# Performance work log

Hardware: AMD Instinct MI355X
Metric: run time of the kernel (lower is better)

Reference implementation:

```python
import jax, jax.numpy as jnp
import numpy as np

B = 65536
DIM = 256       # latent_dim
N_EMBED = 1024  # codebook size


def setup_inputs() -> dict:
    key = jax.random.key(0)
    kx, ke = jax.random.split(key)
    x = jax.random.normal(kx, (B, DIM), dtype=jnp.float32)
    # rosinality Quantize stores codebook as embed[dim, n_embed]
    embed = jax.random.normal(ke, (DIM, N_EMBED), dtype=jnp.float32)
    return {"x": x, "embed": embed}


def reference(x, embed):
    # dist[b, k] = ||x_b||^2 - 2 x_b . e_k + ||e_k||^2  (negated for argmax in
    # the original; equivalent to argmin of the distance)
    x_sq = jnp.sum(x * x, axis=1, keepdims=True)            # [B, 1]
    e_sq = jnp.sum(embed * embed, axis=0, keepdims=True)    # [1, K]
    dist = x_sq - 2.0 * (x @ embed) + e_sq                  # [B, K]
    embed_ind = jnp.argmin(dist, axis=1)                    # [B] int
    # codebook lookup: embed.T is [K, dim]
    quantize = jnp.take(embed.T, embed_ind, axis=0)         # [B, dim]
    # commitment loss term
    diff = jnp.mean(jnp.square(jax.lax.stop_gradient(quantize) - x))
    # straight-through estimator
    quantize_st = x + jax.lax.stop_gradient(quantize - x)
    return quantize_st, diff, embed_ind
```

## Files before the change

### kernel.cpp

```cpp
#include <hip/hip_runtime.h>

#define NROWSQ   65536
#define NDIM     256
#define NCB      1024
#define DIFF_OFF 16777216
#define IDX_OFF  16777217

#define MARGIN_A 0.35f
#define MARGIN_B 1.5e-3f
#define SCORE_SHIFT 384.0f

typedef __attribute__((ext_vector_type(8))) short s16x8;
typedef __attribute__((ext_vector_type(4))) float f32x4;

__device__ __forceinline__ unsigned short f2bf(float f) {
  union { float f; unsigned u; } v; v.f = f;
  return (unsigned short)((v.u + 0x7FFFu + ((v.u >> 16) & 1u)) >> 16);
}

__device__ __forceinline__ void gll16(const void* g, void* l) {
  __builtin_amdgcn_global_load_lds(
      (const __attribute__((address_space(1))) unsigned int*)g,
      (__attribute__((address_space(3))) unsigned int*)l, 16, 0, 0);
}

__device__ __forceinline__ void top2_update(float& v1, int& i1, float& v2, int& i2,
                                            float v, int col) {
  if (v > v1 || (v == v1 && col < i1)) { v2 = v1; i2 = i1; v1 = v; i1 = col; }
  else if (v > v2 || (v == v2 && col < i2)) { v2 = v; i2 = col; }
}
__device__ __forceinline__ void top2_merge(float& v1, int& i1, float& v2, int& i2,
                                           float ov1, int oi1, float ov2, int oi2) {
  if (ov1 > v1 || (ov1 == v1 && oi1 < i1)) {
    float nv2 = v1; int ni2 = i1;
    if (ov2 > nv2 || (ov2 == nv2 && oi2 < ni2)) { nv2 = ov2; ni2 = oi2; }
    v1 = ov1; i1 = oi1; v2 = nv2; i2 = ni2;
  } else if (ov1 > v2 || (ov1 == v2 && oi1 < i2)) {
    v2 = ov1; i2 = oi1;
  }
}

__device__ __forceinline__ float np_pairwise128(const float* p) {
  float r0 = p[0], r1 = p[1], r2 = p[2], r3 = p[3];
  float r4 = p[4], r5 = p[5], r6 = p[6], r7 = p[7];
  for (int i = 8; i < 128; i += 8) {
    r0 += p[i];     r1 += p[i + 1]; r2 += p[i + 2]; r3 += p[i + 3];
    r4 += p[i + 4]; r5 += p[i + 5]; r6 += p[i + 6]; r7 += p[i + 7];
  }
  return ((r0 + r1) + (r2 + r3)) + ((r4 + r5) + (r6 + r7));
}

__global__ void k0a_transpose(const float* __restrict__ E, float* __restrict__ embT,
                              unsigned short* __restrict__ cbT,
                              int* __restrict__ cntA, int* __restrict__ cntB) {
  __shared__ float T[64][65];
  const int t = threadIdx.x;
  const int kbase = (blockIdx.x & 15) * 64;
  const int dbase = (blockIdx.x >> 4) * 64;
  if (blockIdx.x == 0 && t == 0) { *cntA = 0; *cntB = 0; }
  #pragma unroll
  for (int i = 0; i < 4; ++i) {
    const int cid = i * 256 + t;
    const int dl = cid >> 4, kc = cid & 15;
    const float4 v = *(const float4*)(E + (size_t)(dbase + dl) * NCB + kbase + kc * 4);
    T[dl][kc * 4 + 0] = v.x; T[dl][kc * 4 + 1] = v.y;
    T[dl][kc * 4 + 2] = v.z; T[dl][kc * 4 + 3] = v.w;
  }
  __syncthreads();
  #pragma unroll
  for (int i = 0; i < 4; ++i) {
    const int cid = i * 256 + t;
    const int kl = cid >> 4, dc = cid & 15;
    float4 v;
    v.x = T[dc * 4 + 0][kl]; v.y = T[dc * 4 + 1][kl];
    v.z = T[dc * 4 + 2][kl]; v.w = T[dc * 4 + 3][kl];
    *(float4*)(embT + (size_t)(kbase + kl) * NDIM + dbase + dc * 4) = v;
    ushort4 b;
    b.x = f2bf(v.x); b.y = f2bf(v.y); b.z = f2bf(v.z); b.w = f2bf(v.w);
    const int dcol = dbase + dc * 4;
    const int sp = dcol ^ ((kl & 7) << 3);
    *(ushort4*)(cbT + (size_t)(kbase + kl) * NDIM + sp) = b;
  }
}

__global__ void k0b_esq(const float* __restrict__ embT, float* __restrict__ esq32,
                        float* __restrict__ esqs, float* __restrict__ esqr) {
  const int b = blockIdx.x, t = threadIdx.x;
  if (b < 128) {
    const int col = b * 8 + (t >> 5);
    const int l = t & 31;
    double s = 0.0;
    #pragma unroll
    for (int i = 0; i < 8; ++i) {
      const double v = (double)embT[(size_t)col * NDIM + l + i * 32];
      s += v * v;
    }
    #pragma unroll
    for (int m = 16; m >= 1; m >>= 1) s += __shfl_xor(s, m);
    if (l == 0) {
      esq32[col] = (float)(0.5 * s);
      esqs[col] = (float)(0.5 * s) - SCORE_SHIFT;
    }
  } else {
    __shared__ float Ls[16][260];
    const int col0 = (b - 128) * 16;
    #pragma unroll
    for (int i = 0; i < 4; ++i) {
      const int flat = i * 256 + t;
      const int row = flat >> 6, f4 = flat & 63;
      *(float4*)&Ls[row][f4 * 4] =
          *(const float4*)(embT + (size_t)(col0 + row) * NDIM + f4 * 4);
    }
    __syncthreads();
    if (t < 16) {
      float sr = 0.f;
      for (int d = 0; d < NDIM; ++d) {
        const float v = Ls[t][d];
        sr = sr + v * v;
      }
      esqr[col0 + t] = sr;
    }
  }
}

__global__ void k1_scores(
    const float* __restrict__ X, const unsigned short* __restrict__ cbT,
    const float* __restrict__ esqs, int2* __restrict__ part1) {
  __shared__ __align__(16) unsigned short Bs[2][64 * 256];
  __shared__ float esq_l[1024];
  const int t = threadIdx.x;
  const int lane = t & 63, w = t >> 6;
  const int l15 = lane & 15, quad = lane >> 4;
  const int rowbase = blockIdx.x * 128;
  const int swz = (l15 & 7) << 3;

  #pragma unroll
  for (int i = 0; i < 8; ++i)
    gll16(cbT + (size_t)(i * 256 + t) * 8, &Bs[0][(i * 256 + w * 64) * 8]);

  s16x8 afrag[2][8];
  #pragma unroll
  for (int m = 0; m < 2; ++m) {
    const float* xr = X + (size_t)(rowbase + w * 32 + m * 16 + l15) * NDIM;
    #pragma unroll
    for (int ks = 0; ks < 8; ++ks) {
      const float4 xa = *(const float4*)(xr + ks * 32 + quad * 8);
      const float4 xb = *(const float4*)(xr + ks * 32 + quad * 8 + 4);
      s16x8 a;
      a[0] = (short)f2bf(xa.x); a[1] = (short)f2bf(xa.y);
      a[2] = (short)f2bf(xa.z); a[3] = (short)f2bf(xa.w);
      a[4] = (short)f2bf(xb.x); a[5] = (short)f2bf(xb.y);
      a[6] = (short)f2bf(xb.z); a[7] = (short)f2bf(xb.w);
      afrag[m][ks] = a;
    }
  }

  {
    const float4 e4 = *(const float4*)(esqs + t * 4);
    *(float4*)(esq_l + t * 4) = e4;
  }

  int key1[2][4], key2[2][4];
  #pragma unroll
  for (int m = 0; m < 2; ++m)
    #pragma unroll
    for (int r = 0; r < 4; ++r) { key1[m][r] = 0; key2[m][r] = 0; }

  asm volatile("s_waitcnt vmcnt(0)" ::: "memory");
  __syncthreads();

  int cur = 0;
  for (int nt = 0; nt < 16; ++nt) {
    if (nt < 15) {
      const unsigned short* src = cbT + (size_t)(nt + 1) * (64 * 256);
      #pragma unroll
      for (int i = 0; i < 8; ++i)
        gll16(src + (size_t)(i * 256 + t) * 8, &Bs[cur ^ 1][(i * 256 + w * 64) * 8]);
    }

    f32x4 acc[2][4];
    #pragma unroll
    for (int m = 0; m < 2; ++m)
      #pragma unroll
      for (int s = 0; s < 4; ++s) acc[m][s] = (f32x4){0.f, 0.f, 0.f, 0.f};

    #pragma unroll
    for (int ks = 0; ks < 8; ++ks) {
      #pragma unroll
      for (int s = 0; s < 4; ++s) {
        const int us = (s * 16 + l15) * 256 + ((ks * 32 + quad * 8) ^ swz);
        const s16x8 bfr = *(const s16x8*)&Bs[cur][us];
        acc[0][s] = __builtin_amdgcn_mfma_f32_16x16x32_bf16(afrag[0][ks], bfr, acc[0][s], 0, 0, 0);
        acc[1][s] = __builtin_amdgcn_mfma_f32_16x16x32_bf16(afrag[1][ks], bfr, acc[1][s], 0, 0, 0);
      }
    }

    #pragma unroll
    for (int s = 0; s < 4; ++s) {
      const int lcol = nt * 64 + s * 16 + l15;
      const float eq = esq_l[lcol];
      const int suffix = 1023 - lcol;
      #pragma unroll
      for (int m = 0; m < 2; ++m)
        #pragma unroll
        for (int r = 0; r < 4; ++r) {
          float sc = acc[m][s][r] - eq;
          sc = fmaxf(sc, 1.0f);
          const int key = (__float_as_int(sc) & 0xFFFFFC00) | suffix;
          key2[m][r] = max(key2[m][r], min(key1[m][r], key));
          key1[m][r] = max(key1[m][r], key);
        }
    }

    asm volatile("s_waitcnt vmcnt(0)" ::: "memory");
    __syncthreads();
    cur ^= 1;
  }

  #pragma unroll
  for (int mask = 1; mask <= 8; mask <<= 1) {
    #pragma unroll
    for (int m = 0; m < 2; ++m)
      #pragma unroll
      for (int r = 0; r < 4; ++r) {
        const int ok1 = __shfl_xor(key1[m][r], mask);
        const int ok2 = __shfl_xor(key2[m][r], mask);
        const int n1 = max(key1[m][r], ok1);
        const int n2 = max(min(key1[m][r], ok1), max(key2[m][r], ok2));
        key1[m][r] = n1; key2[m][r] = n2;
      }
  }

  if (l15 == 0) {
    #pragma unroll
    for (int m = 0; m < 2; ++m)
      #pragma unroll
      for (int r = 0; r < 4; ++r) {
        const int grow = rowbase + w * 32 + m * 16 + quad * 4 + r;
        part1[grow] = make_int2(key1[m][r], key2[m][r]);
      }
  }
}

__global__ void k1m_merge(const int2* __restrict__ part1, float* __restrict__ outIdx,
                          int* __restrict__ cntA, int* __restrict__ listA,
                          float* __restrict__ outDiff) {
  const int row = blockIdx.x * 256 + threadIdx.x;
  if (row == 0) *outDiff = 0.f;
  const int2 a = part1[row];
  outIdx[row] = (float)(1023 - (a.x & 1023));
  const float g1 = __int_as_float(a.x & 0xFFFFFC00);
  const float g2 = __int_as_float(a.y & 0xFFFFFC00);
  if (g1 - g2 < MARGIN_A) {
    const int p = atomicAdd(cntA, 1);
    listA[p] = row;
  }
}

__global__ __launch_bounds__(256) void k2a_refine(
    const float* __restrict__ X, const float* __restrict__ embT,
    const float* __restrict__ esq, const int* __restrict__ cntA,
    const int* __restrict__ listA, float4* __restrict__ part2) {
  __shared__ float Xs[8][NDIM];
  __shared__ float sv1[4][8], sv2[4][8];
  __shared__ int   si1[4][8], si2[4][8];
  const int t = threadIdx.x;
  const int lane = t & 63, w = t >> 6;
  const int split = blockIdx.x & 3;
  const int col = split * 256 + t;
  const int nslots = gridDim.x >> 2;
  const int cnt = *cntA;
  const float eqc = esq[col];
  const float* er = embT + (size_t)col * NDIM;

  for (int base = (blockIdx.x >> 2) * 8; base < cnt; base += nslots * 8) {
    const int nrows = min(8, cnt - base);
    __syncthreads();
    for (int r = 0; r < 8; ++r) {
      const int rid = listA[base + min(r, nrows - 1)];
      Xs[r][t] = X[(size_t)rid * NDIM + t];
    }
    __syncthreads();

    float acc[8];
    #pragma unroll
    for (int r = 0; r < 8; ++r) acc[r] = 0.f;

    #pragma unroll 4
    for (int dq = 0; dq < 64; ++dq) {
      const float4 e = *(const float4*)(er + dq * 4);
      #pragma unroll
      for (int r = 0; r < 8; ++r) {
        const float4 x = *(const float4*)(&Xs[r][dq * 4]);
        float a = acc[r];
        a = fmaf(x.x, e.x, a);
        a = fmaf(x.y, e.y, a);
        a = fmaf(x.z, e.z, a);
        a = fmaf(x.w, e.w, a);
        acc[r] = a;
      }
    }

    #pragma unroll
    for (int r = 0; r < 8; ++r) {
      float v1 = acc[r] - eqc, v2 = -3.4e38f;
      int   i1 = col, i2 = 0x7fffffff;
      #pragma unroll
      for (int mask = 1; mask < 64; mask <<= 1) {
        const float ov1 = __shfl_xor(v1, mask); const int oi1 = __shfl_xor(i1, mask);
        const float ov2 = __shfl_xor(v2, mask); const int oi2 = __shfl_xor(i2, mask);
        top2_merge(v1, i1, v2, i2, ov1, oi1, ov2, oi2);
      }
      if (lane == 0) { sv1[w][r] = v1; si1[w][r] = i1; sv2[w][r] = v2; si2[w][r] = i2; }
    }
    __syncthreads();
    if (t < nrows) {
      const int r = t;
      float fv1 = sv1[0][r], fv2 = sv2[0][r]; int fi1 = si1[0][r], fi2 = si2[0][r];
      for (int ww = 1; ww < 4; ++ww)
        top2_merge(fv1, fi1, fv2, fi2, sv1[ww][r], si1[ww][r], sv2[ww][r], si2[ww][r]);
      part2[(size_t)split * NROWSQ + base + r] = make_float4(fv1, (float)fi1, fv2, (float)fi2);
    }
    __syncthreads();
  }
}

__global__ void k2m_merge(const float4* __restrict__ part2, const int* __restrict__ cntA,
                          const int* __restrict__ listA, float* __restrict__ outIdx,
                          int* __restrict__ cntB, int* __restrict__ listB) {
  const int cnt = *cntA;
  for (int j = blockIdx.x * 256 + threadIdx.x; j < cnt; j += gridDim.x * 256) {
    const float4 a = part2[j];
    float v1 = a.x, v2 = a.z; int i1 = (int)a.y, i2 = (int)a.w;
    #pragma unroll
    for (int s = 1; s < 4; ++s) {
      const float4 b = part2[(size_t)s * NROWSQ + j];
      top2_merge(v1, i1, v2, i2, b.x, (int)b.y, b.z, (int)b.w);
    }
    const int rid = listA[j];
    outIdx[rid] = (float)i1;
    if (v1 - v2 < MARGIN_B) { const int p = atomicAdd(cntB, 1); listB[p] = rid; }
  }
}

__global__ __launch_bounds__(256) void k2b_mimic(
    const float* __restrict__ X, const float* __restrict__ embT,
    const float* __restrict__ esqr, const int* __restrict__ cntB,
    const int* __restrict__ listB, float* __restrict__ outIdx) {
  __shared__ float Xr[NDIM];
  __shared__ float Psq[NDIM];
  __shared__ float rv[256];
  __shared__ int ri[256];
  const int t = threadIdx.x;
  const int cnt = *cntB;
  for (int j = blockIdx.x; j < cnt; j += gridDim.x) {
    const int rid = listB[j];
    __syncthreads();
    {
      const float x = X[(size_t)rid * NDIM + t];
      Xr[t] = x;
      Psq[t] = x * x;
    }
    __syncthreads();
    const float x_sq = np_pairwise128(Psq) + np_pairwise128(Psq + 128);

    float best = 3.4e38f; int bidx = 0x7fffffff;
    #pragma unroll
    for (int c = 0; c < 4; ++c) {
      const int k = t + c * 256;
      const float* er = embT + (size_t)k * NDIM;
      float acc = 0.f;
      #pragma unroll 8
      for (int dq = 0; dq < 64; ++dq) {
        const float4 e = *(const float4*)(er + dq * 4);
        const float4 x = *(const float4*)(Xr + dq * 4);
        acc = fmaf(x.x, e.x, acc);
        acc = fmaf(x.y, e.y, acc);
        acc = fmaf(x.z, e.z, acc);
        acc = fmaf(x.w, e.w, acc);
      }
      const float dist = (x_sq - 2.0f * acc) + esqr[k];
      if (dist < best || (dist == best && k < bidx)) { best = dist; bidx = k; }
    }
    rv[t] = best; ri[t] = bidx;
    __syncthreads();
    for (int off = 128; off > 0; off >>= 1) {
      if (t < off) {
        if (rv[t + off] < rv[t] || (rv[t + off] == rv[t] && ri[t + off] < ri[t])) {
          rv[t] = rv[t + off]; ri[t] = ri[t + off];
        }
      }
      __syncthreads();
    }
    if (t == 0) outIdx[rid] = (float)ri[0];
  }
}

__global__ __launch_bounds__(256) void k4_outputs(
    const float* __restrict__ X, const float* __restrict__ embT,
    const float* __restrict__ idxF, float* __restrict__ outQ,
    float* __restrict__ outDiff) {
  const int t = threadIdx.x;
  const int lane = t & 63, w = t >> 6;
  const int W = blockIdx.x * 4 + w;
  float s = 0.f;
  #pragma unroll
  for (int i = 0; i < 8; ++i) {
    const int r = W + i * 8192;
    const int idx = (int)idxF[r];
    const float4 q = *(const float4*)(embT + idx * NDIM + lane * 4);
    const float4 x = *(const float4*)(X + (size_t)r * NDIM + lane * 4);
    *(float4*)(outQ + (size_t)r * NDIM + lane * 4) = q;
    const float dx = q.x - x.x, dy = q.y - x.y, dz = q.z - x.z, dw = q.w - x.w;
    s += dx * dx + dy * dy + dz * dz + dw * dw;
  }
  #pragma unroll
  for (int mask = 1; mask < 64; mask <<= 1) s += __shfl_xor(s, mask);
  __shared__ float bs[4];
  if (lane == 0) bs[w] = s;
  __syncthreads();
  if (t == 0)
    atomicAdd(outDiff, (bs[0] + bs[1] + bs[2] + bs[3]) * (1.0f / 16777216.0f));
}

extern "C" void kernel_launch(void* const* d_in, const int* in_sizes, int n_in,
                              void* d_out, int out_size, void* d_ws, size_t ws_size,
                              hipStream_t stream) {
  const float* X = (const float*)d_in[0];
  const float* E = (const float*)d_in[1];
  float* out = (float*)d_out;

  char* ws = (char*)d_ws;
  unsigned short* cbT = (unsigned short*)(ws + 0x000000);
  float*  embT  = (float*) (ws + 0x080000);
  float*  esq32 = (float*) (ws + 0x180000);
  float*  esqs  = (float*) (ws + 0x181000);
  float*  esqr  = (float*) (ws + 0x182000);
  int* cntA  = (int*)(ws + 0x183000);
  int* cntB  = (int*)(ws + 0x183004);
  int* listA = (int*)(ws + 0x183100);
  int* listB = (int*)(ws + 0x1C3100);
  int2*   part1 = (int2*)  (ws + 0x203100);
  float4* part2 = (float4*)(ws + 0x283100);

  float* outQ    = out;
  float* outDiff = out + DIFF_OFF;
  float* outIdx  = out + IDX_OFF;

  k0a_transpose<<<dim3(64), dim3(256), 0, stream>>>(E, embT, cbT, cntA, cntB);
  k0b_esq<<<dim3(192), dim3(256), 0, stream>>>(embT, esq32, esqs, esqr);
  k1_scores<<<dim3(512), dim3(256), 0, stream>>>(X, cbT, esqs, part1);
  k1m_merge<<<dim3(256), dim3(256), 0, stream>>>(part1, outIdx, cntA, listA, outDiff);
  k2a_refine<<<dim3(2048), dim3(256), 0, stream>>>(X, embT, esq32, cntA, listA, part2);
  k2m_merge<<<dim3(64), dim3(256), 0, stream>>>(part2, cntA, listA, outIdx, cntB, listB);
  k2b_mimic<<<dim3(64), dim3(256), 0, stream>>>(X, embT, esqr, cntB, listB, outIdx);
  k4_outputs<<<dim3(2048), dim3(256), 0, stream>>>(X, embT, outIdx, outQ, outDiff);
}
```

Baseline: 343.6 us.

## Track top-3 candidates and refine clear two-way ties with a pair-only check

The bf16 scoring kernel now keeps a top-3 of packed keys per row instead of a top-2. Ambiguous rows whose third candidate falls clearly behind are routed to a new cheap kernel that recomputes only the two leading fp32 dot products. Only the remaining rows go through the full 1024-column refine pass. This cuts the refine workload, at the cost of extra register and shuffle work in the main scoring loop, a wider partial buffer, and one more kernel launch. Correctness now relies on the MARGIN_A3 bound holding for bf16 score error.

```diff
diff --git a/kernel.cpp b/kernel.cpp
--- a/kernel.cpp
+++ b/kernel.cpp
@@ -7,6 +7,7 @@
 #define IDX_OFF  16777217
 
 #define MARGIN_A 0.35f
+#define MARGIN_A3 (MARGIN_A + 0.075f)
 #define MARGIN_B 1.5e-3f
 #define SCORE_SHIFT 384.0f
 
@@ -52,12 +53,12 @@
 
 __global__ void k0a_transpose(const float* __restrict__ E, float* __restrict__ embT,
                               unsigned short* __restrict__ cbT,
-                              int* __restrict__ cntA, int* __restrict__ cntB) {
+                              int* __restrict__ cnts) {
   __shared__ float T[64][65];
   const int t = threadIdx.x;
   const int kbase = (blockIdx.x & 15) * 64;
   const int dbase = (blockIdx.x >> 4) * 64;
-  if (blockIdx.x == 0 && t == 0) { *cntA = 0; *cntB = 0; }
+  if (blockIdx.x == 0 && t < 3) cnts[t] = 0;
   #pragma unroll
   for (int i = 0; i < 4; ++i) {
     const int cid = i * 256 + t;
@@ -125,7 +126,7 @@
 
 __global__ void k1_scores(
     const float* __restrict__ X, const unsigned short* __restrict__ cbT,
-    const float* __restrict__ esqs, int2* __restrict__ part1) {
+    const float* __restrict__ esqs, int4* __restrict__ part1) {
   __shared__ __align__(16) unsigned short Bs[2][64 * 256];
   __shared__ float esq_l[1024];
   const int t = threadIdx.x;
@@ -160,11 +161,11 @@
     *(float4*)(esq_l + t * 4) = e4;
   }
 
-  int key1[2][4], key2[2][4];
+  int key1[2][4], key2[2][4], key3[2][4];
   #pragma unroll
   for (int m = 0; m < 2; ++m)
     #pragma unroll
-    for (int r = 0; r < 4; ++r) { key1[m][r] = 0; key2[m][r] = 0; }
+    for (int r = 0; r < 4; ++r) { key1[m][r] = 0; key2[m][r] = 0; key3[m][r] = 0; }
 
   asm volatile("s_waitcnt vmcnt(0)" ::: "memory");
   __syncthreads();
@@ -207,8 +208,11 @@
           float sc = acc[m][s][r] - eq;
           sc = fmaxf(sc, 1.0f);
           const int key = (__float_as_int(sc) & 0xFFFFFC00) | suffix;
-          key2[m][r] = max(key2[m][r], min(key1[m][r], key));
+          const int tt = min(key1[m][r], key);
+          const int n3 = min(key2[m][r], tt);
           key1[m][r] = max(key1[m][r], key);
+          key2[m][r] = max(key2[m][r], tt);
+          key3[m][r] = max(key3[m][r], n3);
         }
     }
 
@@ -223,11 +227,15 @@
     for (int m = 0; m < 2; ++m)
       #pragma unroll
       for (int r = 0; r < 4; ++r) {
-        const int ok1 = __shfl_xor(key1[m][r], mask);
-        const int ok2 = __shfl_xor(key2[m][r], mask);
-        const int n1 = max(key1[m][r], ok1);
-        const int n2 = max(min(key1[m][r], ok1), max(key2[m][r], ok2));
-        key1[m][r] = n1; key2[m][r] = n2;
+        const int a1 = key1[m][r], a2 = key2[m][r], a3 = key3[m][r];
+        const int b1 = __shfl_xor(a1, mask);
+        const int b2 = __shfl_xor(a2, mask);
+        const int b3 = __shfl_xor(a3, mask);
+        const int p = min(a1, b1);
+        const int q = max(a2, b2);
+        key1[m][r] = max(a1, b1);
+        key2[m][r] = max(p, q);
+        key3[m][r] = max(min(p, q), max(min(a2, b2), max(a3, b3)));
       }
   }
 
@@ -237,30 +245,69 @@
       #pragma unroll
       for (int r = 0; r < 4; ++r) {
         const int grow = rowbase + w * 32 + m * 16 + quad * 4 + r;
-        part1[grow] = make_int2(key1[m][r], key2[m][r]);
-      }
-  }
-}
-
-__global__ void k1m_merge(const int2* __restrict__ part1, float* __restrict__ outIdx,
-                          int* __restrict__ cntA, int* __restrict__ listA,
-                          float* __restrict__ outDiff) {
+        part1[grow] = make_int4(key1[m][r], key2[m][r], key3[m][r], 0);
+      }
+  }
+}
+
+__global__ void k1m_merge(const int4* __restrict__ part1, float* __restrict__ outIdx,
+                          int* __restrict__ cnts, int* __restrict__ listP,
+                          int* __restrict__ listF, float* __restrict__ outDiff) {
   const int row = blockIdx.x * 256 + threadIdx.x;
   if (row == 0) *outDiff = 0.f;
-  const int2 a = part1[row];
+  const int4 a = part1[row];
   outIdx[row] = (float)(1023 - (a.x & 1023));
   const float g1 = __int_as_float(a.x & 0xFFFFFC00);
   const float g2 = __int_as_float(a.y & 0xFFFFFC00);
   if (g1 - g2 < MARGIN_A) {
-    const int p = atomicAdd(cntA, 1);
-    listA[p] = row;
+    const float g3 = __int_as_float(a.z & 0xFFFFFC00);
+    if (g1 - g3 > MARGIN_A3) {
+      const int p = atomicAdd(&cnts[0], 1); listP[p] = row;
+    } else {
+      const int p = atomicAdd(&cnts[1], 1); listF[p] = row;
+    }
+  }
+}
+
+__global__ __launch_bounds__(256) void k2p_pair(
+    const float* __restrict__ X, const float* __restrict__ embT,
+    const float* __restrict__ esq32, const int* __restrict__ cnts,
+    const int* __restrict__ listP, const int4* __restrict__ part1,
+    float* __restrict__ outIdx, int* __restrict__ cntB, int* __restrict__ listB) {
+  const int cnt = cnts[0];
+  for (int j = blockIdx.x * 256 + threadIdx.x; j < cnt; j += gridDim.x * 256) {
+    const int rid = listP[j];
+    const int4 k = part1[rid];
+    const int c1 = 1023 - (k.x & 1023);
+    const int c2 = 1023 - (k.y & 1023);
+    const float* xr = X + (size_t)rid * NDIM;
+    const float* e1 = embT + (size_t)c1 * NDIM;
+    const float* e2 = embT + (size_t)c2 * NDIM;
+    float a1 = 0.f, a2 = 0.f;
+    #pragma unroll 4
+    for (int dq = 0; dq < 64; ++dq) {
+      const float4 x = *(const float4*)(xr + dq * 4);
+      const float4 p = *(const float4*)(e1 + dq * 4);
+      const float4 q = *(const float4*)(e2 + dq * 4);
+      a1 = fmaf(x.x, p.x, a1); a1 = fmaf(x.y, p.y, a1);
+      a1 = fmaf(x.z, p.z, a1); a1 = fmaf(x.w, p.w, a1);
+      a2 = fmaf(x.x, q.x, a2); a2 = fmaf(x.y, q.y, a2);
+      a2 = fmaf(x.z, q.z, a2); a2 = fmaf(x.w, q.w, a2);
+    }
+    const float s1 = a1 - esq32[c1];
+    const float s2 = a2 - esq32[c2];
+    float v1, v2; int i1, i2;
+    if (s1 > s2 || (s1 == s2 && c1 < c2)) { v1 = s1; i1 = c1; v2 = s2; i2 = c2; }
+    else                                  { v1 = s2; i1 = c2; v2 = s1; i2 = c1; }
+    outIdx[rid] = (float)i1;
+    if (v1 - v2 < MARGIN_B) { const int p = atomicAdd(cntB, 1); listB[p] = rid; }
   }
 }
 
 __global__ __launch_bounds__(256) void k2a_refine(
     const float* __restrict__ X, const float* __restrict__ embT,
-    const float* __restrict__ esq, const int* __restrict__ cntA,
-    const int* __restrict__ listA, float4* __restrict__ part2) {
+    const float* __restrict__ esq, const int* __restrict__ cnts,
+    const int* __restrict__ listF, float4* __restrict__ part2) {
   __shared__ float Xs[8][NDIM];
   __shared__ float sv1[4][8], sv2[4][8];
   __shared__ int   si1[4][8], si2[4][8];
@@ -269,7 +316,7 @@
   const int split = blockIdx.x & 3;
   const int col = split * 256 + t;
   const int nslots = gridDim.x >> 2;
-  const int cnt = *cntA;
+  const int cnt = cnts[1];
   const float eqc = esq[col];
   const float* er = embT + (size_t)col * NDIM;
 
@@ -277,7 +324,7 @@
     const int nrows = min(8, cnt - base);
     __syncthreads();
     for (int r = 0; r < 8; ++r) {
-      const int rid = listA[base + min(r, nrows - 1)];
+      const int rid = listF[base + min(r, nrows - 1)];
       Xs[r][t] = X[(size_t)rid * NDIM + t];
     }
     __syncthreads();
@@ -325,10 +372,10 @@
   }
 }
 
-__global__ void k2m_merge(const float4* __restrict__ part2, const int* __restrict__ cntA,
-                          const int* __restrict__ listA, float* __restrict__ outIdx,
+__global__ void k2m_merge(const float4* __restrict__ part2, const int* __restrict__ cnts,
+                          const int* __restrict__ listF, float* __restrict__ outIdx,
                           int* __restrict__ cntB, int* __restrict__ listB) {
-  const int cnt = *cntA;
+  const int cnt = cnts[1];
   for (int j = blockIdx.x * 256 + threadIdx.x; j < cnt; j += gridDim.x * 256) {
     const float4 a = part2[j];
     float v1 = a.x, v2 = a.z; int i1 = (int)a.y, i2 = (int)a.w;
@@ -337,7 +384,7 @@
       const float4 b = part2[(size_t)s * NROWSQ + j];
       top2_merge(v1, i1, v2, i2, b.x, (int)b.y, b.z, (int)b.w);
     }
-    const int rid = listA[j];
+    const int rid = listF[j];
     outIdx[rid] = (float)i1;
     if (v1 - v2 < MARGIN_B) { const int p = atomicAdd(cntB, 1); listB[p] = rid; }
   }
@@ -436,23 +483,27 @@
   float*  esq32 = (float*) (ws + 0x180000);
   float*  esqs  = (float*) (ws + 0x181000);
   float*  esqr  = (float*) (ws + 0x182000);
-  int* cntA  = (int*)(ws + 0x183000);
-  int* cntB  = (int*)(ws + 0x183004);
-  int* listA = (int*)(ws + 0x183100);
-  int* listB = (int*)(ws + 0x1C3100);
-  int2*   part1 = (int2*)  (ws + 0x203100);
-  float4* part2 = (float4*)(ws + 0x283100);
+  int* cnts  = (int*)(ws + 0x183000);
+  int* listP = (int*)(ws + 0x183100);
+  int* listF = (int*)(ws + 0x1C3100);
+  int* listB = (int*)(ws + 0x203100);
+  int4*   part1 = (int4*)  (ws + 0x243100);
+  float4* part2 = (float4*)(ws + 0x343100);
+
+  int* cntB = cnts + 2;
 
   float* outQ    = out;
   float* outDiff = out + DIFF_OFF;
   float* outIdx  = out + IDX_OFF;
 
-  k0a_transpose<<<dim3(64), dim3(256), 0, stream>>>(E, embT, cbT, cntA, cntB);
+  k0a_transpose<<<dim3(64), dim3(256), 0, stream>>>(E, embT, cbT, cnts);
   k0b_esq<<<dim3(192), dim3(256), 0, stream>>>(embT, esq32, esqs, esqr);
   k1_scores<<<dim3(512), dim3(256), 0, stream>>>(X, cbT, esqs, part1);
-  k1m_merge<<<dim3(256), dim3(256), 0, stream>>>(part1, outIdx, cntA, listA, outDiff);
-  k2a_refine<<<dim3(2048), dim3(256), 0, stream>>>(X, embT, esq32, cntA, listA, part2);
-  k2m_merge<<<dim3(64), dim3(256), 0, stream>>>(part2, cntA, listA, outIdx, cntB, listB);
+  k1m_merge<<<dim3(256), dim3(256), 0, stream>>>(part1, outIdx, cnts, listP, listF, outDiff);
+  k2p_pair<<<dim3(256), dim3(256), 0, stream>>>(X, embT, esq32, cnts, listP, part1,
+                                                outIdx, cntB, listB);
+  k2a_refine<<<dim3(2048), dim3(256), 0, stream>>>(X, embT, esq32, cnts, listF, part2);
+  k2m_merge<<<dim3(64), dim3(256), 0, stream>>>(part2, cnts, listF, outIdx, cntB, listB);
   k2b_mimic<<<dim3(64), dim3(256), 0, stream>>>(X, embT, esqr, cntB, listB, outIdx);
   k4_outputs<<<dim3(2048), dim3(256), 0, stream>>>(X, embT, outIdx, outQ, outDiff);
 }
```

New measurement: 360.4 us. +4.9%, slower.
